# Optimization experiments

Measured on AMD Instinct MI355X. Metric: run time of the kernel, lower is better.

Reference implementation:

```python
import jax, jax.numpy as jnp
import numpy as np

N_NODES = 100000
N_EDGES = 2000000
D = 128
REL_TYPES = 64


def setup_inputs() -> dict:
    key = jax.random.key(0)
    k1, k2, k3, k4 = jax.random.split(key, 4)
    z = jax.random.normal(k1, (N_NODES, D), dtype=jnp.float32)
    edge_index = jax.random.randint(k2, (2, N_EDGES), 0, N_NODES, dtype=jnp.int64)
    rel_id = jax.random.randint(k3, (N_EDGES,), 0, REL_TYPES, dtype=jnp.int64)
    rel = jax.random.normal(k4, (REL_TYPES, D), dtype=jnp.float32)
    return {"z": z, "edge_index": edge_index, "rel_id": rel_id, "rel": rel}


def reference(z, edge_index, rel_id, rel):
    # DistMult: sigmoid(sum_d z[src,d] * rel[rel_id,d] * z[dst,d])
    src = z[edge_index[0]]          # [E, D]
    dst = z[edge_index[1]]          # [E, D]
    r = rel[rel_id]                 # [E, D]
    scores = jnp.sum(src * r * dst, axis=1)  # [E]
    return jax.nn.sigmoid(scores)
```

## Files before the change

### kernel.cpp

```cpp
#include <hip/hip_runtime.h>
#include <hip/hip_bf16.h>
#include <hip/hip_fp16.h>


__global__ __launch_bounds__(256) void convert_kernel(
    const float* __restrict__ z, __half* __restrict__ zh, int n8)
{
    const int i = blockIdx.x * blockDim.x + threadIdx.x;
    if (i >= n8) return;
    const float4 f0 = ((const float4*)z)[2 * i];
    const float4 f1 = ((const float4*)z)[2 * i + 1];
    union { __half2 h2[4]; uint4 u; } o;
    o.h2[0] = __floats2half2_rn(f0.x, f0.y);
    o.h2[1] = __floats2half2_rn(f0.z, f0.w);
    o.h2[2] = __floats2half2_rn(f1.x, f1.y);
    o.h2[3] = __floats2half2_rn(f1.z, f1.w);
    ((uint4*)zh)[i] = o.u;
}

__global__ __launch_bounds__(256) void distmult_f16_kernel(
    const __half* __restrict__ zh,
    const int* __restrict__ src_idx,
    const int* __restrict__ dst_idx,
    const int* __restrict__ rel_id,
    const float* __restrict__ rel,
    float* __restrict__ out,
    int E)
{
    const int gtid = blockIdx.x * blockDim.x + threadIdx.x;
    const int e    = gtid >> 4;
    const int lane = threadIdx.x & 15;
    if (e >= E) return;

    const int s = src_idx[e];
    const int d = dst_idx[e];
    const int r = rel_id[e];

    union { uint4 u; __half2 h2[4]; } A, B;
    A.u = ((const uint4*)(zh + (size_t)s * 128))[lane];
    B.u = ((const uint4*)(zh + (size_t)d * 128))[lane];
    const float4* rr = (const float4*)(rel + (size_t)r * 128);
    const float4 r0 = rr[2 * lane];
    const float4 r1 = rr[2 * lane + 1];

    const float2 a0 = __half22float2(A.h2[0]);
    const float2 a1 = __half22float2(A.h2[1]);
    const float2 a2 = __half22float2(A.h2[2]);
    const float2 a3 = __half22float2(A.h2[3]);
    const float2 b0 = __half22float2(B.h2[0]);
    const float2 b1 = __half22float2(B.h2[1]);
    const float2 b2 = __half22float2(B.h2[2]);
    const float2 b3 = __half22float2(B.h2[3]);

    float v = a0.x * r0.x * b0.x
            + a0.y * r0.y * b0.y
            + a1.x * r0.z * b1.x
            + a1.y * r0.w * b1.y
            + a2.x * r1.x * b2.x
            + a2.y * r1.y * b2.y
            + a3.x * r1.z * b3.x
            + a3.y * r1.w * b3.y;

    #pragma unroll
    for (int off = 8; off > 0; off >>= 1)
        v += __shfl_down(v, off, 16);

    if (lane == 0)
        out[e] = 1.0f / (1.0f + __expf(-v));
}

__global__ __launch_bounds__(256) void distmult_f32_kernel(
    const float* __restrict__ z,
    const int* __restrict__ src_idx,
    const int* __restrict__ dst_idx,
    const int* __restrict__ rel_id,
    const float* __restrict__ rel,
    float* __restrict__ out,
    int E)
{
    const int gtid = blockIdx.x * blockDim.x + threadIdx.x;
    const int e    = gtid >> 4;
    const int lane = threadIdx.x & 15;
    if (e >= E) return;

    const int s = src_idx[e];
    const int d = dst_idx[e];
    const int r = rel_id[e];

    const float4* zs = (const float4*)(z   + (size_t)s * 128);
    const float4* zd = (const float4*)(z   + (size_t)d * 128);
    const float4* rr = (const float4*)(rel + (size_t)r * 128);

    const float4 a0 = zs[lane];
    const float4 a1 = zs[lane + 16];
    const float4 b0 = zd[lane];
    const float4 b1 = zd[lane + 16];
    const float4 c0 = rr[lane];
    const float4 c1 = rr[lane + 16];

    float v = a0.x * c0.x * b0.x + a0.y * c0.y * b0.y
            + a0.z * c0.z * b0.z + a0.w * c0.w * b0.w
            + a1.x * c1.x * b1.x + a1.y * c1.y * b1.y
            + a1.z * c1.z * b1.z + a1.w * c1.w * b1.w;

    #pragma unroll
    for (int off = 8; off > 0; off >>= 1)
        v += __shfl_down(v, off, 16);

    if (lane == 0)
        out[e] = 1.0f / (1.0f + __expf(-v));
}

extern "C" void kernel_launch(void* const* d_in, const int* in_sizes, int n_in,
                              void* d_out, int out_size, void* d_ws, size_t ws_size,
                              hipStream_t stream) {
    const float* z       = (const float*)d_in[0];
    const int*   eidx    = (const int*)d_in[1];
    const int*   rel_id  = (const int*)d_in[2];
    const float* rel     = (const float*)d_in[3];
    float*       out     = (float*)d_out;

    const int nz = in_sizes[0];
    const int E  = in_sizes[2];
    const int* src_idx = eidx;
    const int* dst_idx = eidx + E;

    const int threads = 256;
    const int edges_per_block = threads / 16;
    const int blocks = (E + edges_per_block - 1) / edges_per_block;

    const size_t need = (size_t)nz * sizeof(__half);
    if (ws_size >= need) {
        __half* zh = (__half*)d_ws;
        const int n8 = nz / 8;
        convert_kernel<<<(n8 + threads - 1) / threads, threads, 0, stream>>>(z, zh, n8);
        distmult_f16_kernel<<<blocks, threads, 0, stream>>>(
            zh, src_idx, dst_idx, rel_id, rel, out, E);
    } else {
        distmult_f32_kernel<<<blocks, threads, 0, stream>>>(
            z, src_idx, dst_idx, rel_id, rel, out, E);
    }
}
```

Before: 229.4 us.

## Bin edges by source-node range before gathering to improve cache locality

Adds a histogram, scan and scatter pipeline that sorts edges into 8 buckets by source-node range. The edges are packed as 64-bit src/dst/rel/id words, and the gather kernel then runs over the bucketed edges. The aim is to make concurrent gathers of fp16 z rows touch a narrower address range and so hit the cache more. In exchange it adds three extra kernels and roughly 40MB of extra index traffic. The grid for each bucket is capped at E/8 + E/64 + 1024 edges, which is only correct when source indices are close to uniformly distributed.

```diff
diff --git a/kernel.cpp b/kernel.cpp
--- a/kernel.cpp
+++ b/kernel.cpp
@@ -1,7 +1,10 @@
 #include <hip/hip_runtime.h>
-#include <hip/hip_bf16.h>
 #include <hip/hip_fp16.h>
-
+#include <stdint.h>
+
+
+#define HIST_BLOCKS 1024
+#define BLOCK 256
 
 __global__ __launch_bounds__(256) void convert_kernel(
     const float* __restrict__ z, __half* __restrict__ zh, int n8)
@@ -18,23 +21,111 @@
     ((uint4*)zh)[i] = o.u;
 }
 
-__global__ __launch_bounds__(256) void distmult_f16_kernel(
+__device__ __forceinline__ uint32_t bucket_of(uint32_t s, uint32_t nn) {
+    uint32_t b = (s * 8u) / nn;
+    return b > 7u ? 7u : b;
+}
+
+__global__ __launch_bounds__(256) void hist_kernel(
+    const int* __restrict__ src, int E, int nn, uint32_t* __restrict__ blockcounts)
+{
+    __shared__ uint32_t cnt[8];
+    if (threadIdx.x < 8) cnt[threadIdx.x] = 0;
+    __syncthreads();
+    for (int i = blockIdx.x * BLOCK + threadIdx.x; i < E; i += HIST_BLOCKS * BLOCK) {
+        uint32_t b = bucket_of((uint32_t)src[i], (uint32_t)nn);
+        atomicAdd(&cnt[b], 1u);
+    }
+    __syncthreads();
+    if (threadIdx.x < 8)
+        blockcounts[blockIdx.x * 8 + threadIdx.x] = cnt[threadIdx.x];
+}
+
+__global__ __launch_bounds__(256) void scan_kernel(
+    const uint32_t* __restrict__ blockcounts,
+    uint32_t* __restrict__ blockbase,
+    uint32_t* __restrict__ bucketbase,
+    uint32_t* __restrict__ bucketcount,
+    int E)
+{
+    const int t = threadIdx.x;
+    const int NPT = (8 * HIST_BLOCKS) / 256;
+    uint32_t local[NPT];
+    uint32_t sum = 0;
+    #pragma unroll
+    for (int k = 0; k < NPT; k++) {
+        int lin = t * NPT + k;
+        int b = lin >> 10, blk = lin & (HIST_BLOCKS - 1);
+        local[k] = sum;
+        sum += blockcounts[blk * 8 + b];
+    }
+    __shared__ uint32_t part[256];
+    part[t] = sum;
+    __syncthreads();
+    for (int off = 1; off < 256; off <<= 1) {
+        uint32_t v = (t >= off) ? part[t - off] : 0;
+        __syncthreads();
+        part[t] += v;
+        __syncthreads();
+    }
+    const uint32_t excl = part[t] - sum;
+    __shared__ uint32_t bb[8];
+    #pragma unroll
+    for (int k = 0; k < NPT; k++) {
+        int lin = t * NPT + k;
+        int b = lin >> 10, blk = lin & (HIST_BLOCKS - 1);
+        uint32_t base = excl + local[k];
+        blockbase[blk * 8 + b] = base;
+        if (blk == 0) bb[b] = base;
+    }
+    __syncthreads();
+    if (t < 8) {
+        bucketbase[t] = bb[t];
+        uint32_t nb = (t < 7) ? bb[t + 1] : (uint32_t)E;
+        bucketcount[t] = nb - bb[t];
+    }
+}
+
+__global__ __launch_bounds__(256) void scatter_kernel(
+    const int* __restrict__ src, const int* __restrict__ dst,
+    const int* __restrict__ relid, int E, int nn,
+    const uint32_t* __restrict__ blockbase, uint64_t* __restrict__ binned)
+{
+    __shared__ uint32_t cur[8];
+    if (threadIdx.x < 8) cur[threadIdx.x] = blockbase[blockIdx.x * 8 + threadIdx.x];
+    __syncthreads();
+    for (int i = blockIdx.x * BLOCK + threadIdx.x; i < E; i += HIST_BLOCKS * BLOCK) {
+        uint32_t s = (uint32_t)src[i];
+        uint32_t d = (uint32_t)dst[i];
+        uint32_t r = (uint32_t)relid[i];
+        uint32_t b = bucket_of(s, (uint32_t)nn);
+        uint32_t pos = atomicAdd(&cur[b], 1u);
+        binned[pos] = (uint64_t)s | ((uint64_t)d << 17)
+                    | ((uint64_t)r << 34) | ((uint64_t)i << 40);
+    }
+}
+
+__global__ __launch_bounds__(256) void distmult_binned_kernel(
     const __half* __restrict__ zh,
-    const int* __restrict__ src_idx,
-    const int* __restrict__ dst_idx,
-    const int* __restrict__ rel_id,
+    const uint64_t* __restrict__ binned,
+    const uint32_t* __restrict__ bucketbase,
+    const uint32_t* __restrict__ bucketcount,
     const float* __restrict__ rel,
-    float* __restrict__ out,
-    int E)
-{
-    const int gtid = blockIdx.x * blockDim.x + threadIdx.x;
-    const int e    = gtid >> 4;
-    const int lane = threadIdx.x & 15;
-    if (e >= E) return;
-
-    const int s = src_idx[e];
-    const int d = dst_idx[e];
-    const int r = rel_id[e];
+    float* __restrict__ out)
+{
+    const int bkt   = blockIdx.x & 7;
+    const int chunk = blockIdx.x >> 3;
+    const int g     = threadIdx.x >> 4;
+    const int lane  = threadIdx.x & 15;
+    const uint32_t cnt = bucketcount[bkt];
+    const uint32_t el  = (uint32_t)chunk * 16u + (uint32_t)g;
+    if (el >= cnt) return;
+
+    const uint64_t p = binned[bucketbase[bkt] + el];
+    const uint32_t s   = (uint32_t)p & 0x1FFFFu;
+    const uint32_t d   = (uint32_t)(p >> 17) & 0x1FFFFu;
+    const uint32_t r   = (uint32_t)(p >> 34) & 0x3Fu;
+    const uint32_t eid = (uint32_t)(p >> 40);
 
     union { uint4 u; __half2 h2[4]; } A, B;
     A.u = ((const uint4*)(zh + (size_t)s * 128))[lane];
@@ -52,92 +143,130 @@
     const float2 b2 = __half22float2(B.h2[2]);
     const float2 b3 = __half22float2(B.h2[3]);
 
-    float v = a0.x * r0.x * b0.x
-            + a0.y * r0.y * b0.y
-            + a1.x * r0.z * b1.x
-            + a1.y * r0.w * b1.y
-            + a2.x * r1.x * b2.x
-            + a2.y * r1.y * b2.y
-            + a3.x * r1.z * b3.x
-            + a3.y * r1.w * b3.y;
+    float v = a0.x * r0.x * b0.x + a0.y * r0.y * b0.y
+            + a1.x * r0.z * b1.x + a1.y * r0.w * b1.y
+            + a2.x * r1.x * b2.x + a2.y * r1.y * b2.y
+            + a3.x * r1.z * b3.x + a3.y * r1.w * b3.y;
 
     #pragma unroll
     for (int off = 8; off > 0; off >>= 1)
         v += __shfl_down(v, off, 16);
 
     if (lane == 0)
-        out[e] = 1.0f / (1.0f + __expf(-v));
+        out[eid] = 1.0f / (1.0f + __expf(-v));
+}
+
+__global__ __launch_bounds__(256) void distmult_f16_kernel(
+    const __half* __restrict__ zh,
+    const int* __restrict__ src_idx, const int* __restrict__ dst_idx,
+    const int* __restrict__ rel_id, const float* __restrict__ rel,
+    float* __restrict__ out, int E)
+{
+    const int gtid = blockIdx.x * blockDim.x + threadIdx.x;
+    const int e = gtid >> 4;
+    const int lane = threadIdx.x & 15;
+    if (e >= E) return;
+    const int s = src_idx[e], d = dst_idx[e], r = rel_id[e];
+    union { uint4 u; __half2 h2[4]; } A, B;
+    A.u = ((const uint4*)(zh + (size_t)s * 128))[lane];
+    B.u = ((const uint4*)(zh + (size_t)d * 128))[lane];
+    const float4* rr = (const float4*)(rel + (size_t)r * 128);
+    const float4 r0 = rr[2 * lane];
+    const float4 r1 = rr[2 * lane + 1];
+    const float2 a0 = __half22float2(A.h2[0]), a1 = __half22float2(A.h2[1]);
+    const float2 a2 = __half22float2(A.h2[2]), a3 = __half22float2(A.h2[3]);
+    const float2 b0 = __half22float2(B.h2[0]), b1 = __half22float2(B.h2[1]);
+    const float2 b2 = __half22float2(B.h2[2]), b3 = __half22float2(B.h2[3]);
+    float v = a0.x * r0.x * b0.x + a0.y * r0.y * b0.y
+            + a1.x * r0.z * b1.x + a1.y * r0.w * b1.y
+            + a2.x * r1.x * b2.x + a2.y * r1.y * b2.y
+            + a3.x * r1.z * b3.x + a3.y * r1.w * b3.y;
+    #pragma unroll
+    for (int off = 8; off > 0; off >>= 1) v += __shfl_down(v, off, 16);
+    if (lane == 0) out[e] = 1.0f / (1.0f + __expf(-v));
 }
 
 __global__ __launch_bounds__(256) void distmult_f32_kernel(
     const float* __restrict__ z,
-    const int* __restrict__ src_idx,
-    const int* __restrict__ dst_idx,
-    const int* __restrict__ rel_id,
-    const float* __restrict__ rel,
-    float* __restrict__ out,
-    int E)
+    const int* __restrict__ src_idx, const int* __restrict__ dst_idx,
+    const int* __restrict__ rel_id, const float* __restrict__ rel,
+    float* __restrict__ out, int E)
 {
     const int gtid = blockIdx.x * blockDim.x + threadIdx.x;
-    const int e    = gtid >> 4;
+    const int e = gtid >> 4;
     const int lane = threadIdx.x & 15;
     if (e >= E) return;
-
-    const int s = src_idx[e];
-    const int d = dst_idx[e];
-    const int r = rel_id[e];
-
-    const float4* zs = (const float4*)(z   + (size_t)s * 128);
-    const float4* zd = (const float4*)(z   + (size_t)d * 128);
+    const int s = src_idx[e], d = dst_idx[e], r = rel_id[e];
+    const float4* zs = (const float4*)(z + (size_t)s * 128);
+    const float4* zd = (const float4*)(z + (size_t)d * 128);
     const float4* rr = (const float4*)(rel + (size_t)r * 128);
-
-    const float4 a0 = zs[lane];
-    const float4 a1 = zs[lane + 16];
-    const float4 b0 = zd[lane];
-    const float4 b1 = zd[lane + 16];
-    const float4 c0 = rr[lane];
-    const float4 c1 = rr[lane + 16];
-
+    const float4 a0 = zs[lane], a1 = zs[lane + 16];
+    const float4 b0 = zd[lane], b1 = zd[lane + 16];
+    const float4 c0 = rr[lane], c1 = rr[lane + 16];
     float v = a0.x * c0.x * b0.x + a0.y * c0.y * b0.y
             + a0.z * c0.z * b0.z + a0.w * c0.w * b0.w
             + a1.x * c1.x * b1.x + a1.y * c1.y * b1.y
             + a1.z * c1.z * b1.z + a1.w * c1.w * b1.w;
-
-    #pragma unroll
-    for (int off = 8; off > 0; off >>= 1)
-        v += __shfl_down(v, off, 16);
-
-    if (lane == 0)
-        out[e] = 1.0f / (1.0f + __expf(-v));
+    #pragma unroll
+    for (int off = 8; off > 0; off >>= 1) v += __shfl_down(v, off, 16);
+    if (lane == 0) out[e] = 1.0f / (1.0f + __expf(-v));
 }
 
 extern "C" void kernel_launch(void* const* d_in, const int* in_sizes, int n_in,
                               void* d_out, int out_size, void* d_ws, size_t ws_size,
                               hipStream_t stream) {
-    const float* z       = (const float*)d_in[0];
-    const int*   eidx    = (const int*)d_in[1];
-    const int*   rel_id  = (const int*)d_in[2];
-    const float* rel     = (const float*)d_in[3];
-    float*       out     = (float*)d_out;
+    const float* z      = (const float*)d_in[0];
+    const int*   eidx   = (const int*)d_in[1];
+    const int*   relid  = (const int*)d_in[2];
+    const float* rel    = (const float*)d_in[3];
+    float*       out    = (float*)d_out;
 
     const int nz = in_sizes[0];
     const int E  = in_sizes[2];
-    const int* src_idx = eidx;
-    const int* dst_idx = eidx + E;
-
-    const int threads = 256;
-    const int edges_per_block = threads / 16;
-    const int blocks = (E + edges_per_block - 1) / edges_per_block;
-
-    const size_t need = (size_t)nz * sizeof(__half);
-    if (ws_size >= need) {
+    const int nn = nz / 128;
+    const int* src = eidx;
+    const int* dst = eidx + E;
+
+    const size_t sz_zh      = (size_t)nz * sizeof(__half);
+    const size_t off_binned = (sz_zh + 255) & ~(size_t)255;
+    const size_t sz_binned  = (size_t)E * 8;
+    const size_t off_bc     = off_binned + sz_binned;
+    const size_t sz_bc      = (size_t)HIST_BLOCKS * 8 * 4;
+    const size_t off_bb     = off_bc + sz_bc;
+    const size_t off_bkb    = off_bb + sz_bc;
+    const size_t off_bkc    = off_bkb + 64;
+    const size_t need       = off_bkc + 64;
+
+    const bool bits_ok = (nn <= 131072) && (E <= (1 << 21)) && (nz % 8 == 0);
+
+    if (ws_size >= need && bits_ok) {
+        char* ws = (char*)d_ws;
+        __half*   zh          = (__half*)(ws);
+        uint64_t* binned      = (uint64_t*)(ws + off_binned);
+        uint32_t* blockcounts = (uint32_t*)(ws + off_bc);
+        uint32_t* blockbase   = (uint32_t*)(ws + off_bb);
+        uint32_t* bucketbase  = (uint32_t*)(ws + off_bkb);
+        uint32_t* bucketcount = (uint32_t*)(ws + off_bkc);
+
+        const int n8 = nz / 8;
+        convert_kernel<<<(n8 + 255) / 256, 256, 0, stream>>>(z, zh, n8);
+        hist_kernel<<<HIST_BLOCKS, BLOCK, 0, stream>>>(src, E, nn, blockcounts);
+        scan_kernel<<<1, 256, 0, stream>>>(blockcounts, blockbase,
+                                           bucketbase, bucketcount, E);
+        scatter_kernel<<<HIST_BLOCKS, BLOCK, 0, stream>>>(src, dst, relid, E, nn,
+                                                          blockbase, binned);
+        const int cap_edges = E / 8 + E / 64 + 1024;
+        const int nblk_per  = (cap_edges + 15) / 16;
+        distmult_binned_kernel<<<8 * nblk_per, 256, 0, stream>>>(
+            zh, binned, bucketbase, bucketcount, rel, out);
+    } else if (ws_size >= sz_zh && nz % 8 == 0) {
         __half* zh = (__half*)d_ws;
         const int n8 = nz / 8;
-        convert_kernel<<<(n8 + threads - 1) / threads, threads, 0, stream>>>(z, zh, n8);
-        distmult_f16_kernel<<<blocks, threads, 0, stream>>>(
-            zh, src_idx, dst_idx, rel_id, rel, out, E);
+        convert_kernel<<<(n8 + 255) / 256, 256, 0, stream>>>(z, zh, n8);
+        const int blocks = (E * 16 + 255) / 256;
+        distmult_f16_kernel<<<blocks, 256, 0, stream>>>(zh, src, dst, relid, rel, out, E);
     } else {
-        distmult_f32_kernel<<<blocks, threads, 0, stream>>>(
-            z, src_idx, dst_idx, rel_id, rel, out, E);
-    }
-}
+        const int blocks = (E * 16 + 255) / 256;
+        distmult_f32_kernel<<<blocks, 256, 0, stream>>>(z, src, dst, relid, rel, out, E);
+    }
+}
```

Result: slower. 241.6 us (+5.3%).
